# Kernel tuning notes

Measured on AMD Instinct MI355X. Metric: run time of the kernel, lower is better.

## Reference

```python
import jax, jax.numpy as jnp
import numpy as np

B, T, I, H = 64, 512, 1024, 2048


def setup_inputs() -> dict:
    key = jax.random.key(0)
    ks = jax.random.split(key, 6)
    s = 1.0 / np.sqrt(H).astype(np.float32)
    return {
        "input": jax.random.normal(ks[0], (B, T, I), jnp.float32),
        "internal": jax.random.normal(ks[1], (B, T), jnp.float32) * 0.1,
        "w_ih": jax.random.uniform(ks[2], (H, I), jnp.float32, -s, s),
        "w_hh": jax.random.uniform(ks[3], (H, H), jnp.float32, -s, s),
        "b_ih": jax.random.uniform(ks[4], (H,), jnp.float32, -s, s),
        "b_hh": jax.random.uniform(ks[5], (H,), jnp.float32, -s, s),
        "h0": jnp.zeros((1, B, H), jnp.float32),
        "trunc": 64,
    }


def reference(input, internal, w_ih, w_hh, b_ih, b_hh, h0, trunc):
    # input: [B, T, I]; internal: [B, T] scalar-per-step drive; h0: [1, B, H]
    Tlen = input.shape[1]
    # Hoist the input projection out of the recurrence (same math, one big GEMM).
    x_proj = jnp.einsum('bti,hi->bth', input, w_ih) + b_ih  # [B, T, H]
    # Truncated-BPTT boundaries: state is detached when i % trunc == 0.
    detach_mask = (jnp.arange(Tlen) % trunc) == 0  # [T] bool

    def step(h, xs):
        xp, noise, m = xs  # xp: [B, H], noise: [B], m: scalar bool
        # detach state at truncation boundary (no-op in forward pass)
        h = jnp.where(m, jax.lax.stop_gradient(h), h)
        h_new = jnp.tanh(xp + noise[:, None] + h @ w_hh.T + b_hh)
        return h_new, h_new

    h_last, outs = jax.lax.scan(
        step, h0[0], (x_proj.transpose(1, 0, 2), internal.T, detach_mask))
    # outputs: [B, T, H], final state: [1, B, H]
    return outs.transpose(1, 0, 2), h_last[None]
```

## Files before the change

### kernel.cpp

```cpp
#include <hip/hip_runtime.h>
#include <hip/hip_bf16.h>
#include <math.h>

#define Bb 64
#define Tt 512
#define Ii 1024
#define Hh 2048
#define NBLK 128

typedef __attribute__((ext_vector_type(8))) short bf16x8;
typedef __attribute__((ext_vector_type(8))) unsigned short ushort8;
typedef __attribute__((ext_vector_type(4))) float f32x4;

__device__ __forceinline__ unsigned short f2bf(float x) {
    unsigned int u = __float_as_uint(x);
    unsigned int r = u + 0x7fffu + ((u >> 16) & 1u);
    return (unsigned short)(r >> 16);
}

__global__ __launch_bounds__(256) void cvt_kernel(
    const float* __restrict__ src, unsigned short* __restrict__ dst)
{
    const int i = (blockIdx.x * 256 + threadIdx.x) * 4;
    float4 v = *(const float4*)(src + i);
    ushort4 o;
    o.x = f2bf(v.x); o.y = f2bf(v.y); o.z = f2bf(v.z); o.w = f2bf(v.w);
    *(ushort4*)(dst + i) = o;
}

__global__ void init_flags(unsigned int* flags) {
    if (threadIdx.x <= NBLK) flags[threadIdx.x] = 0u;
}

__global__ __launch_bounds__(256, 2) void xproj_kernel(
    const float* __restrict__ A,
    const unsigned short* __restrict__ Wbf,
    const float* __restrict__ bias,
    float* __restrict__ out)
{
    __shared__ unsigned short As[128 * 40];
    __shared__ unsigned short Bs[128 * 40];

    const int tid  = threadIdx.x;
    const int lane = tid & 63;
    const int wid  = tid >> 6;
    const int wm   = wid & 1;
    const int wn   = wid >> 1;
    const int rlo  = lane & 15;
    const int khi  = lane >> 4;

    const int m0 = blockIdx.y * 128;
    const int n0 = blockIdx.x * 128;

    f32x4 acc[4][4];
    #pragma unroll
    for (int i = 0; i < 4; ++i)
        #pragma unroll
        for (int j = 0; j < 4; ++j) acc[i][j] = (f32x4)0.f;

    for (int k0 = 0; k0 < Ii; k0 += 32) {
        #pragma unroll
        for (int p = 0; p < 4; ++p) {
            const int flat = p * 256 + tid;
            const int row  = flat >> 3;
            const int c4   = flat & 7;
            float4 v = *(const float4*)(A + (size_t)(m0 + row) * Ii + k0 + c4 * 4);
            ushort4 o;
            o.x = f2bf(v.x); o.y = f2bf(v.y); o.z = f2bf(v.z); o.w = f2bf(v.w);
            *(ushort4*)(As + row * 40 + c4 * 4) = o;
        }
        #pragma unroll
        for (int p = 0; p < 2; ++p) {
            const int flat = p * 256 + tid;
            const int row  = flat >> 2;
            const int c8   = flat & 3;
            ushort8 v = *(const ushort8*)(Wbf + (size_t)(n0 + row) * Ii + k0 + c8 * 8);
            *(ushort8*)(Bs + row * 40 + c8 * 8) = v;
        }
        __syncthreads();

        bf16x8 af[4], bfr[4];
        #pragma unroll
        for (int i = 0; i < 4; ++i)
            af[i] = *(const bf16x8*)(As + (wm * 64 + i * 16 + rlo) * 40 + khi * 8);
        #pragma unroll
        for (int j = 0; j < 4; ++j)
            bfr[j] = *(const bf16x8*)(Bs + (wn * 64 + j * 16 + rlo) * 40 + khi * 8);
        #pragma unroll
        for (int i = 0; i < 4; ++i)
            #pragma unroll
            for (int j = 0; j < 4; ++j)
                acc[i][j] = __builtin_amdgcn_mfma_f32_16x16x32_bf16(
                    af[i], bfr[j], acc[i][j], 0, 0, 0);
        __syncthreads();
    }

    #pragma unroll
    for (int j = 0; j < 4; ++j) {
        const int col = n0 + wn * 64 + j * 16 + rlo;
        const float bj = bias[col];
        #pragma unroll
        for (int i = 0; i < 4; ++i) {
            #pragma unroll
            for (int r = 0; r < 4; ++r) {
                const int m = m0 + wm * 64 + i * 16 + khi * 4 + r;
                out[(size_t)m * Hh + col] = acc[i][j][r] + bj;
            }
        }
    }
}

#define LD_FRAG(dst, base, OFF)                                               \
    asm volatile("global_load_dwordx4 %0, %1, off offset:" OFF " sc0 sc1"     \
                 : "=v"(dst) : "v"(base))

#define DRAIN16(a)                                                            \
    asm volatile("s_waitcnt vmcnt(0)"                                         \
                 : "+v"(a[0][0]), "+v"(a[0][1]), "+v"(a[0][2]), "+v"(a[0][3]),\
                   "+v"(a[0][4]), "+v"(a[0][5]), "+v"(a[0][6]), "+v"(a[0][7]),\
                   "+v"(a[1][0]), "+v"(a[1][1]), "+v"(a[1][2]), "+v"(a[1][3]),\
                   "+v"(a[1][4]), "+v"(a[1][5]), "+v"(a[1][6]), "+v"(a[1][7]) \
                 :: "memory");                                                \
    __builtin_amdgcn_sched_barrier(0)

#define RAW_BARRIER()                                                         \
    asm volatile("s_waitcnt lgkmcnt(0)\n\ts_barrier" ::: "memory")

__global__ __launch_bounds__(512, 1) void rnn_persistent(
    const unsigned short* __restrict__ w_bf,
    unsigned short* __restrict__ h_bf,
    const float* __restrict__ b_hh,
    const float* __restrict__ internal,
    float* __restrict__ out,
    unsigned int* __restrict__ flags)
{
    __shared__ f32x4 red4[8 * 256];

    const int tid  = threadIdx.x;
    const int lane = tid & 63;
    const int wid  = tid >> 6;
    const int rlo  = lane & 15;
    const int khi  = lane >> 4;
    const int blk  = blockIdx.x;
    const int rh   = blk & 1;
    const int cg   = blk >> 1;
    unsigned int* root = flags + NBLK;

    bf16x8 wf[2][8];
    #pragma unroll
    for (int nt = 0; nt < 2; ++nt) {
        const unsigned short* wrow =
            w_bf + (size_t)(cg * 32 + nt * 16 + rlo) * Hh + wid * 256 + khi * 8;
        #pragma unroll
        for (int kit = 0; kit < 8; ++kit)
            wf[nt][kit] = *(const bf16x8*)(wrow + kit * 32);
    }

    const int em    = (tid >> 6) & 1;
    const int ent   = (tid >> 7) & 1;
    const int odd   = lane & 1;
    const int clloc = (ent * 16 + rlo) & ~1;
    const int cl    = cg * 32 + clloc;
    const int rAl   = em * 16 + khi * 4 + 2 * odd;
    const int rAg   = rh * 32 + rAl;
    const int rBg   = rAg + 1;
    const float2 bh2 = (tid < 256) ? *(const float2*)(b_hh + cl)
                                   : make_float2(0.f, 0.f);

    float2 xpA = make_float2(0.f, 0.f), xpB = make_float2(0.f, 0.f);
    float  nzA = 0.f, nzB = 0.f;
    if (tid < 256) {
        xpA = *(const float2*)(out + ((size_t)rAg * Tt + 0) * Hh + cl);
        xpB = *(const float2*)(out + ((size_t)rBg * Tt + 0) * Hh + cl);
        nzA = internal[rAg * Tt + 0];
        nzB = internal[rBg * Tt + 0];
    }
    float2 gA_d = make_float2(0.f, 0.f), gB_d = make_float2(0.f, 0.f);

    for (int t = 0; t < Tt; ++t) {
        const bool last = (t == Tt - 1);
        const unsigned short* h_cur = h_bf + (size_t)(t & 1) * Bb * Hh;
        unsigned short*       h_nxt = h_bf + (size_t)((t + 1) & 1) * Bb * Hh;

        const unsigned short* am0 =
            h_cur + (size_t)(rh * 32 + rlo) * Hh + wid * 256 + khi * 8;
        const unsigned short* am1 = am0 + (size_t)16 * Hh;

        bf16x8 a[2][8];
        LD_FRAG(a[0][0], am0, "0");   LD_FRAG(a[0][1], am0, "64");
        LD_FRAG(a[0][2], am0, "128"); LD_FRAG(a[0][3], am0, "192");
        LD_FRAG(a[0][4], am0, "256"); LD_FRAG(a[0][5], am0, "320");
        LD_FRAG(a[0][6], am0, "384"); LD_FRAG(a[0][7], am0, "448");
        LD_FRAG(a[1][0], am1, "0");   LD_FRAG(a[1][1], am1, "64");
        LD_FRAG(a[1][2], am1, "128"); LD_FRAG(a[1][3], am1, "192");
        LD_FRAG(a[1][4], am1, "256"); LD_FRAG(a[1][5], am1, "320");
        LD_FRAG(a[1][6], am1, "384"); LD_FRAG(a[1][7], am1, "448");

        if (tid < 256 && t > 0) {
            *(float2*)(out + ((size_t)rAg * Tt + (t - 1)) * Hh + cl) = gA_d;
            *(float2*)(out + ((size_t)rBg * Tt + (t - 1)) * Hh + cl) = gB_d;
        }

        DRAIN16(a);

        f32x4 acc[2][2];
        #pragma unroll
        for (int m = 0; m < 2; ++m)
            #pragma unroll
            for (int nt = 0; nt < 2; ++nt) acc[m][nt] = (f32x4)0.f;
        #pragma unroll
        for (int kk = 0; kk < 8; ++kk)
            #pragma unroll
            for (int m = 0; m < 2; ++m)
                #pragma unroll
                for (int nt = 0; nt < 2; ++nt)
                    acc[m][nt] = __builtin_amdgcn_mfma_f32_16x16x32_bf16(
                        a[m][kk], wf[nt][kk], acc[m][nt], 0, 0, 0);

        #pragma unroll
        for (int nt = 0; nt < 2; ++nt)
            #pragma unroll
            for (int m = 0; m < 2; ++m)
                red4[wid * 256 + (nt * 2 + m) * 64 + lane] = acc[m][nt];
        RAW_BARRIER();

        if (tid < 256) {
            f32x4 s4 = (f32x4)0.f;
            #pragma unroll
            for (int ks = 0; ks < 8; ++ks)
                s4 += red4[ks * 256 + tid];

            f32x4 o4;
            #pragma unroll
            for (int i = 0; i < 4; ++i)
                o4[i] = __shfl_xor(s4[i], 1, 64);

            const float sA_lo = odd ? o4[2] : s4[0];
            const float sA_hi = odd ? s4[2] : o4[0];
            const float sB_lo = odd ? o4[3] : s4[1];
            const float sB_hi = odd ? s4[3] : o4[1];

            float2 gA, gB;
            gA.x = tanhf(xpA.x + nzA + bh2.x + sA_lo);
            gA.y = tanhf(xpA.y + nzA + bh2.y + sA_hi);
            gB.x = tanhf(xpB.x + nzB + bh2.x + sB_lo);
            gB.y = tanhf(xpB.y + nzB + bh2.y + sB_hi);

            const unsigned int hpA =
                (unsigned int)f2bf(gA.x) | ((unsigned int)f2bf(gA.y) << 16);
            const unsigned int hpB =
                (unsigned int)f2bf(gB.x) | ((unsigned int)f2bf(gB.y) << 16);
            __hip_atomic_store((unsigned int*)h_nxt + ((size_t)rAg * Hh + cl) / 2,
                               hpA, __ATOMIC_RELAXED, __HIP_MEMORY_SCOPE_AGENT);
            __hip_atomic_store((unsigned int*)h_nxt + ((size_t)rBg * Hh + cl) / 2,
                               hpB, __ATOMIC_RELAXED, __HIP_MEMORY_SCOPE_AGENT);

            if (last) {
                *(float2*)(out + ((size_t)rAg * Tt + t) * Hh + cl) = gA;
                *(float2*)(out + ((size_t)rBg * Tt + t) * Hh + cl) = gB;
                float* tail = out + (size_t)Bb * Tt * Hh;
                *(float2*)(tail + (size_t)rAg * Hh + cl) = gA;
                *(float2*)(tail + (size_t)rBg * Hh + cl) = gB;
            } else {
                gA_d = gA; gB_d = gB;
            }
        }
        if (last) break;

        asm volatile("s_waitcnt vmcnt(0)" ::: "memory");

        if (tid < 256) {
            xpA = *(const float2*)(out + ((size_t)rAg * Tt + t + 1) * Hh + cl);
            xpB = *(const float2*)(out + ((size_t)rBg * Tt + t + 1) * Hh + cl);
            nzA = internal[rAg * Tt + t + 1];
            nzB = internal[rBg * Tt + t + 1];
        }

        RAW_BARRIER();

        if (tid == 0)
            __hip_atomic_store(flags + blk, (unsigned int)(t + 1),
                               __ATOMIC_RELAXED, __HIP_MEMORY_SCOPE_AGENT);

        const unsigned int tgt = (unsigned int)(t + 1);
        if (blk == 0 && wid == 7) {
            while (true) {
                unsigned int f0 = __hip_atomic_load(
                    flags + lane, __ATOMIC_RELAXED, __HIP_MEMORY_SCOPE_AGENT);
                unsigned int f1 = __hip_atomic_load(
                    flags + 64 + lane, __ATOMIC_RELAXED, __HIP_MEMORY_SCOPE_AGENT);
                if (__all((f0 >= tgt) && (f1 >= tgt))) break;
                __builtin_amdgcn_s_sleep(1);
            }
            if (lane == 0)
                __hip_atomic_store(root, tgt, __ATOMIC_RELAXED,
                                   __HIP_MEMORY_SCOPE_AGENT);
        } else if (wid == 7) {
            while (__hip_atomic_load(root, __ATOMIC_RELAXED,
                                     __HIP_MEMORY_SCOPE_AGENT) < tgt)
                __builtin_amdgcn_s_sleep(1);
        }
        RAW_BARRIER();
    }
}

extern "C" void kernel_launch(void* const* d_in, const int* in_sizes, int n_in,
                              void* d_out, int out_size, void* d_ws, size_t ws_size,
                              hipStream_t stream) {
    const float* input    = (const float*)d_in[0];
    const float* internal = (const float*)d_in[1];
    const float* w_ih     = (const float*)d_in[2];
    const float* w_hh     = (const float*)d_in[3];
    const float* b_ih     = (const float*)d_in[4];
    const float* b_hh     = (const float*)d_in[5];
    const float* h0       = (const float*)d_in[6];
    float* out = (float*)d_out;

    unsigned short* w_hh_bf = (unsigned short*)d_ws;
    unsigned short* w_ih_bf = w_hh_bf + (size_t)Hh * Hh;
    unsigned short* h_bf    = w_ih_bf + (size_t)Hh * Ii;
    unsigned int*   flags   = (unsigned int*)(h_bf + (size_t)2 * Bb * Hh);

    hipLaunchKernelGGL(init_flags, dim3(1), dim3(256), 0, stream, flags);
    hipLaunchKernelGGL(cvt_kernel, dim3((Hh * Hh) / 1024), dim3(256), 0, stream,
                       w_hh, w_hh_bf);
    hipLaunchKernelGGL(cvt_kernel, dim3((Hh * Ii) / 1024), dim3(256), 0, stream,
                       w_ih, w_ih_bf);
    hipLaunchKernelGGL(cvt_kernel, dim3((Bb * Hh) / 1024), dim3(256), 0, stream,
                       h0, h_bf);

    dim3 g1(Hh / 128, (Bb * Tt) / 128);
    hipLaunchKernelGGL(xproj_kernel, g1, dim3(256), 0, stream,
                       input, w_ih_bf, b_ih, out);

    void* args[] = {(void*)&w_hh_bf, (void*)&h_bf, (void*)&b_hh,
                    (void*)&internal, (void*)&out, (void*)&flags};
    hipLaunchCooperativeKernel((void*)rnn_persistent, dim3(NBLK), dim3(512),
                               args, 0, stream);
}
```

Measured before the change: 4.045 ms.

## Replace centralized grid barrier with per-wave flag waits and triple-buffered state

```diff
diff --git a/kernel.cpp b/kernel.cpp
--- a/kernel.cpp
+++ b/kernel.cpp
@@ -29,7 +29,7 @@
 }
 
 __global__ void init_flags(unsigned int* flags) {
-    if (threadIdx.x <= NBLK) flags[threadIdx.x] = 0u;
+    flags[threadIdx.x] = 0u;
 }
 
 __global__ __launch_bounds__(256, 2) void xproj_kernel(
@@ -126,7 +126,9 @@
 #define RAW_BARRIER()                                                         \
     asm volatile("s_waitcnt lgkmcnt(0)\n\ts_barrier" ::: "memory")
 
-__global__ __launch_bounds__(512, 1) void rnn_persistent(
+__global__ __launch_bounds__(512)
+__attribute__((amdgpu_waves_per_eu(2, 2)))
+void rnn_persistent(
     const unsigned short* __restrict__ w_bf,
     unsigned short* __restrict__ h_bf,
     const float* __restrict__ b_hh,
@@ -134,7 +136,7 @@
     float* __restrict__ out,
     unsigned int* __restrict__ flags)
 {
-    __shared__ f32x4 red4[8 * 256];
+    __shared__ f32x4 red4[2][8 * 256];
 
     const int tid  = threadIdx.x;
     const int lane = tid & 63;
@@ -144,7 +146,6 @@
     const int blk  = blockIdx.x;
     const int rh   = blk & 1;
     const int cg   = blk >> 1;
-    unsigned int* root = flags + NBLK;
 
     bf16x8 wf[2][8];
     #pragma unroll
@@ -155,6 +156,11 @@
         for (int kit = 0; kit < 8; ++kit)
             wf[nt][kit] = *(const bf16x8*)(wrow + kit * 32);
     }
+
+    const int pcg  = wid * 8 + (lane & 7);
+    const int prh  = (lane >> 3) & 1;
+    const int pw   = (lane >> 4) & 3;
+    const int fidx = ((pcg * 2 + prh) << 2) + pw;
 
     const int em    = (tid >> 6) & 1;
     const int ent   = (tid >> 7) & 1;
@@ -179,8 +185,18 @@
 
     for (int t = 0; t < Tt; ++t) {
         const bool last = (t == Tt - 1);
-        const unsigned short* h_cur = h_bf + (size_t)(t & 1) * Bb * Hh;
-        unsigned short*       h_nxt = h_bf + (size_t)((t + 1) & 1) * Bb * Hh;
+        const unsigned short* h_cur = h_bf + (size_t)(t % 3) * Bb * Hh;
+        unsigned short*       h_nxt = h_bf + (size_t)((t + 1) % 3) * Bb * Hh;
+
+        {
+            const unsigned int tgt = (unsigned int)t;
+            while (true) {
+                unsigned int f = __hip_atomic_load(
+                    flags + fidx, __ATOMIC_RELAXED, __HIP_MEMORY_SCOPE_AGENT);
+                if (__all(f >= tgt)) break;
+                __builtin_amdgcn_s_sleep(1);
+            }
+        }
 
         const unsigned short* am0 =
             h_cur + (size_t)(rh * 32 + rlo) * Hh + wid * 256 + khi * 8;
@@ -217,18 +233,19 @@
                     acc[m][nt] = __builtin_amdgcn_mfma_f32_16x16x32_bf16(
                         a[m][kk], wf[nt][kk], acc[m][nt], 0, 0, 0);
 
+        f32x4* rb = red4[t & 1];
         #pragma unroll
         for (int nt = 0; nt < 2; ++nt)
             #pragma unroll
             for (int m = 0; m < 2; ++m)
-                red4[wid * 256 + (nt * 2 + m) * 64 + lane] = acc[m][nt];
+                rb[wid * 256 + (nt * 2 + m) * 64 + lane] = acc[m][nt];
         RAW_BARRIER();
 
         if (tid < 256) {
             f32x4 s4 = (f32x4)0.f;
             #pragma unroll
             for (int ks = 0; ks < 8; ++ks)
-                s4 += red4[ks * 256 + tid];
+                s4 += rb[ks * 256 + tid];
 
             f32x4 o4;
             #pragma unroll
@@ -263,44 +280,19 @@
                 *(float2*)(tail + (size_t)rBg * Hh + cl) = gB;
             } else {
                 gA_d = gA; gB_d = gB;
+
+                asm volatile("s_waitcnt vmcnt(0)" ::: "memory");
+                if (lane == 0)
+                    __hip_atomic_store(flags + blk * 4 + wid,
+                                       (unsigned int)(t + 1),
+                                       __ATOMIC_RELAXED, __HIP_MEMORY_SCOPE_AGENT);
+
+                xpA = *(const float2*)(out + ((size_t)rAg * Tt + t + 1) * Hh + cl);
+                xpB = *(const float2*)(out + ((size_t)rBg * Tt + t + 1) * Hh + cl);
+                nzA = internal[rAg * Tt + t + 1];
+                nzB = internal[rBg * Tt + t + 1];
             }
         }
-        if (last) break;
-
-        asm volatile("s_waitcnt vmcnt(0)" ::: "memory");
-
-        if (tid < 256) {
-            xpA = *(const float2*)(out + ((size_t)rAg * Tt + t + 1) * Hh + cl);
-            xpB = *(const float2*)(out + ((size_t)rBg * Tt + t + 1) * Hh + cl);
-            nzA = internal[rAg * Tt + t + 1];
-            nzB = internal[rBg * Tt + t + 1];
-        }
-
-        RAW_BARRIER();
-
-        if (tid == 0)
-            __hip_atomic_store(flags + blk, (unsigned int)(t + 1),
-                               __ATOMIC_RELAXED, __HIP_MEMORY_SCOPE_AGENT);
-
-        const unsigned int tgt = (unsigned int)(t + 1);
-        if (blk == 0 && wid == 7) {
-            while (true) {
-                unsigned int f0 = __hip_atomic_load(
-                    flags + lane, __ATOMIC_RELAXED, __HIP_MEMORY_SCOPE_AGENT);
-                unsigned int f1 = __hip_atomic_load(
-                    flags + 64 + lane, __ATOMIC_RELAXED, __HIP_MEMORY_SCOPE_AGENT);
-                if (__all((f0 >= tgt) && (f1 >= tgt))) break;
-                __builtin_amdgcn_s_sleep(1);
-            }
-            if (lane == 0)
-                __hip_atomic_store(root, tgt, __ATOMIC_RELAXED,
-                                   __HIP_MEMORY_SCOPE_AGENT);
-        } else if (wid == 7) {
-            while (__hip_atomic_load(root, __ATOMIC_RELAXED,
-                                     __HIP_MEMORY_SCOPE_AGENT) < tgt)
-                __builtin_amdgcn_s_sleep(1);
-        }
-        RAW_BARRIER();
     }
 }
 
@@ -319,9 +311,9 @@
     unsigned short* w_hh_bf = (unsigned short*)d_ws;
     unsigned short* w_ih_bf = w_hh_bf + (size_t)Hh * Hh;
     unsigned short* h_bf    = w_ih_bf + (size_t)Hh * Ii;
-    unsigned int*   flags   = (unsigned int*)(h_bf + (size_t)2 * Bb * Hh);
-
-    hipLaunchKernelGGL(init_flags, dim3(1), dim3(256), 0, stream, flags);
+    unsigned int*   flags   = (unsigned int*)(h_bf + (size_t)3 * Bb * Hh);
+
+    hipLaunchKernelGGL(init_flags, dim3(1), dim3(512), 0, stream, flags);
     hipLaunchKernelGGL(cvt_kernel, dim3((Hh * Hh) / 1024), dim3(256), 0, stream,
                        w_hh, w_hh_bf);
     hipLaunchKernelGGL(cvt_kernel, dim3((Hh * Ii) / 1024), dim3(256), 0, stream,
```

Measured after the change: 4.209 ms. 1.04x slower.

## Split grid barrier into two independent row-half barriers, batch weight loads

Applied to the files above, without the earlier changes.

```diff
diff --git a/kernel.cpp b/kernel.cpp
--- a/kernel.cpp
+++ b/kernel.cpp
@@ -29,7 +29,7 @@
 }
 
 __global__ void init_flags(unsigned int* flags) {
-    if (threadIdx.x <= NBLK) flags[threadIdx.x] = 0u;
+    if (threadIdx.x < NBLK + 2) flags[threadIdx.x] = 0u;
 }
 
 __global__ __launch_bounds__(256, 2) void xproj_kernel(
@@ -114,6 +114,10 @@
     asm volatile("global_load_dwordx4 %0, %1, off offset:" OFF " sc0 sc1"     \
                  : "=v"(dst) : "v"(base))
 
+#define LD_FRAG_C(dst, base, OFF)                                             \
+    asm volatile("global_load_dwordx4 %0, %1, off offset:" OFF                \
+                 : "=v"(dst) : "v"(base))
+
 #define DRAIN16(a)                                                            \
     asm volatile("s_waitcnt vmcnt(0)"                                         \
                  : "+v"(a[0][0]), "+v"(a[0][1]), "+v"(a[0][2]), "+v"(a[0][3]),\
@@ -126,7 +130,7 @@
 #define RAW_BARRIER()                                                         \
     asm volatile("s_waitcnt lgkmcnt(0)\n\ts_barrier" ::: "memory")
 
-__global__ __launch_bounds__(512, 1) void rnn_persistent(
+__global__ __launch_bounds__(512, 2) void rnn_persistent(
     const unsigned short* __restrict__ w_bf,
     unsigned short* __restrict__ h_bf,
     const float* __restrict__ b_hh,
@@ -144,16 +148,21 @@
     const int blk  = blockIdx.x;
     const int rh   = blk & 1;
     const int cg   = blk >> 1;
-    unsigned int* root = flags + NBLK;
 
     bf16x8 wf[2][8];
-    #pragma unroll
-    for (int nt = 0; nt < 2; ++nt) {
-        const unsigned short* wrow =
-            w_bf + (size_t)(cg * 32 + nt * 16 + rlo) * Hh + wid * 256 + khi * 8;
-        #pragma unroll
-        for (int kit = 0; kit < 8; ++kit)
-            wf[nt][kit] = *(const bf16x8*)(wrow + kit * 32);
+    {
+        const unsigned short* w0 =
+            w_bf + (size_t)(cg * 32 + rlo) * Hh + wid * 256 + khi * 8;
+        const unsigned short* w1 = w0 + (size_t)16 * Hh;
+        LD_FRAG_C(wf[0][0], w0, "0");   LD_FRAG_C(wf[0][1], w0, "64");
+        LD_FRAG_C(wf[0][2], w0, "128"); LD_FRAG_C(wf[0][3], w0, "192");
+        LD_FRAG_C(wf[0][4], w0, "256"); LD_FRAG_C(wf[0][5], w0, "320");
+        LD_FRAG_C(wf[0][6], w0, "384"); LD_FRAG_C(wf[0][7], w0, "448");
+        LD_FRAG_C(wf[1][0], w1, "0");   LD_FRAG_C(wf[1][1], w1, "64");
+        LD_FRAG_C(wf[1][2], w1, "128"); LD_FRAG_C(wf[1][3], w1, "192");
+        LD_FRAG_C(wf[1][4], w1, "256"); LD_FRAG_C(wf[1][5], w1, "320");
+        LD_FRAG_C(wf[1][6], w1, "384"); LD_FRAG_C(wf[1][7], w1, "448");
+        DRAIN16(wf);
     }
 
     const int em    = (tid >> 6) & 1;
@@ -283,20 +292,19 @@
                                __ATOMIC_RELAXED, __HIP_MEMORY_SCOPE_AGENT);
 
         const unsigned int tgt = (unsigned int)(t + 1);
-        if (blk == 0 && wid == 7) {
+        if (blk < 2 && wid == 7) {
             while (true) {
-                unsigned int f0 = __hip_atomic_load(
-                    flags + lane, __ATOMIC_RELAXED, __HIP_MEMORY_SCOPE_AGENT);
-                unsigned int f1 = __hip_atomic_load(
-                    flags + 64 + lane, __ATOMIC_RELAXED, __HIP_MEMORY_SCOPE_AGENT);
-                if (__all((f0 >= tgt) && (f1 >= tgt))) break;
+                unsigned int f = __hip_atomic_load(
+                    flags + lane * 2 + blk, __ATOMIC_RELAXED,
+                    __HIP_MEMORY_SCOPE_AGENT);
+                if (__all(f >= tgt)) break;
                 __builtin_amdgcn_s_sleep(1);
             }
             if (lane == 0)
-                __hip_atomic_store(root, tgt, __ATOMIC_RELAXED,
+                __hip_atomic_store(flags + NBLK + blk, tgt, __ATOMIC_RELAXED,
                                    __HIP_MEMORY_SCOPE_AGENT);
         } else if (wid == 7) {
-            while (__hip_atomic_load(root, __ATOMIC_RELAXED,
+            while (__hip_atomic_load(flags + NBLK + rh, __ATOMIC_RELAXED,
                                      __HIP_MEMORY_SCOPE_AGENT) < tgt)
                 __builtin_amdgcn_s_sleep(1);
         }
```

Measured after the change: 3.957 ms. 1.02x faster.
